# Kernel tuning notes

Hardware: AMD Instinct MI355X
Metric: run time of the kernel (lower is better)

## Reference

```python
import jax, jax.numpy as jnp
import numpy as np

B = 8           # hardcoded batchsize in the original forward
EPS = 1e-4      # scn.BatchNormalization default eps


def setup_inputs() -> dict:
    key = jax.random.key(0)
    ks = jax.random.split(key, 8)
    Nq, Nkv = 16384, 32768
    dec_in, enc_in, nf = 64, 64, 128
    nbr = jax.random.randint(ks[2], (Nq, 27), 0, Nq, dtype=jnp.int32)
    # center tap of the 3x3x3 submanifold conv is the point itself
    nbr = nbr.at[:, 13].set(jnp.arange(Nq, dtype=jnp.int32))
    return {
        "x_decoder_feat": jax.random.normal(ks[0], (Nq, dec_in), jnp.float32),
        "x_encoder_feat": jax.random.normal(ks[1], (Nkv, enc_in), jnp.float32),
        "nbr_idx": nbr,
        "W_p1": jax.random.normal(ks[3], (27, dec_in, nf), jnp.float32) * 0.05,
        "W_q": jax.random.normal(ks[4], (nf, nf), jnp.float32) * 0.05,
        "W_k": jax.random.normal(ks[5], (enc_in, nf), jnp.float32) * 0.05,
        "W_v": jax.random.normal(ks[6], (enc_in, nf), jnp.float32) * 0.05,
        "W_trans": jax.random.normal(ks[7], (nf, nf), jnp.float32) * 0.05,
        "gamma": jnp.ones((nf,), jnp.float32),
        "beta": jnp.zeros((nf,), jnp.float32),
    }


def reference(x_decoder_feat, x_encoder_feat, nbr_idx, W_p1, W_q, W_k, W_v,
              W_trans, gamma, beta):
    nf = W_q.shape[1]
    # p1: 3x3x3 submanifold conv = gather 27 neighbors, per-offset matmul, sum
    x_dec = jnp.einsum('nkc,kcf->nf', x_decoder_feat[nbr_idx], W_p1)  # [Nq,nf]
    q = (x_dec @ W_q).reshape(B, -1, nf)            # [B, nq, nf]
    k = (x_encoder_feat @ W_k).reshape(B, -1, nf)   # [B, nkv, nf]
    v = (x_encoder_feat @ W_v).reshape(B, -1, nf)
    # per-batch QK^T softmax V (no 1/sqrt(d) scaling in original)
    attn = jax.nn.softmax(jnp.einsum('bqc,bkc->bqk', q, k), axis=-1)
    x_r = jnp.einsum('bqk,bkc->bqc', attn, v).reshape(-1, nf)  # [Nq,nf]
    # trans_conv (1x1) + batchnorm (batch stats over all points)
    t = x_r @ W_trans
    mean = t.mean(axis=0)
    var = t.var(axis=0)
    bn = (t - mean) * jax.lax.rsqrt(var + EPS) * gamma + beta
    return x_dec + bn
```

## Files before the change

kernel.cpp:

```cpp
#include <hip/hip_runtime.h>
#include <math.h>

#define NQ      16384
#define NKV     32768
#define CIN     64
#define NF      128
#define NOFF    27
#define BATCH   8
#define SQ      2048
#define SKV     4096
#define BN_EPS  1e-4f
#define SPLIT   4
#define KV_PER_SPLIT (SKV / SPLIT)
#define TILES_PER_SPLIT (KV_PER_SPLIT / 64)

typedef unsigned short u16;
typedef __attribute__((ext_vector_type(4))) float f32x4;
typedef __attribute__((ext_vector_type(8))) short s16x8;

__device__ __forceinline__ u16 f2b(float x) {
    union { float f; unsigned u; } c; c.f = x;
    unsigned r = (c.u + 0x7FFFu + ((c.u >> 16) & 1u)) >> 16;
    return (u16)r;
}
__device__ __forceinline__ float b2f(u16 x) {
    union { unsigned u; float f; } c; c.u = ((unsigned)x) << 16;
    return c.f;
}
__device__ __forceinline__ void g2l16(const void* gp, void* lp) {
    __builtin_amdgcn_global_load_lds(
        (const __attribute__((address_space(1))) unsigned*)gp,
        (__attribute__((address_space(3))) unsigned*)lp, 16, 0, 0);
}

__global__ __launch_bounds__(256) void cvt_bf16_kernel(
    const float* __restrict__ src, u16* __restrict__ dst)
{
    int i = (blockIdx.x * 256 + threadIdx.x) * 4;
    float4 v = *(const float4*)(src + i);
    ushort4 o;
    o.x = f2b(v.x); o.y = f2b(v.y); o.z = f2b(v.z); o.w = f2b(v.w);
    *(ushort4*)(dst + i) = o;
}

__global__ __launch_bounds__(256) void cvt_wp1t_kernel(
    const float* __restrict__ src, u16* __restrict__ dst)
{
    int id = blockIdx.x * 256 + threadIdx.x;
    int ko = id >> 11;
    int r  = id & 2047;
    int f  = r >> 4;
    int c4 = (r & 15) * 4;
    const float* s = src + (size_t)ko * 8192 + (size_t)c4 * NF + f;
    ushort4 o;
    o.x = f2b(s[0]); o.y = f2b(s[NF]); o.z = f2b(s[2 * NF]); o.w = f2b(s[3 * NF]);
    *(ushort4*)(dst + (size_t)ko * 8192 + (size_t)f * 64 + c4) = o;
}

__global__ __launch_bounds__(256, 3) void p1conv_mfma_kernel(
    const u16* __restrict__ xf, const int* __restrict__ nbr,
    const u16* __restrict__ wt, float* __restrict__ out)
{
    __shared__ u16 As[64][64];
    __shared__ u16 Bs[64][64];
    __shared__ int nbr_s[64][28];

    const int t    = threadIdx.x;
    const int w    = t >> 6;
    const int lane = t & 63;
    const int quad = lane >> 4;
    const int l15  = lane & 15;
    const int base = blockIdx.x * 64;
    const int fh   = blockIdx.y;

    for (int i = t; i < 64 * NOFF; i += 256)
        nbr_s[i / NOFF][i % NOFF] = nbr[(size_t)base * NOFF + i];

    f32x4 oacc[4];
    #pragma unroll
    for (int n = 0; n < 4; n++) oacc[n] = (f32x4)0.f;

    __syncthreads();

    for (int ko = 0; ko < NOFF; ko++) {
        if (ko) __syncthreads();
        #pragma unroll
        for (int c = 0; c < 2; c++) {
            int row = w * 16 + c * 8 + (lane >> 3);
            int k8  = (lane & 7) ^ (row & 7);
            int nb  = nbr_s[row][ko];
            g2l16(xf + (size_t)nb * CIN + k8 * 8, &As[w * 16 + c * 8][0]);
        }
        #pragma unroll
        for (int c = 0; c < 2; c++) {
            int row = w * 16 + c * 8 + (lane >> 3);
            int k8  = (lane & 7) ^ (row & 7);
            g2l16(wt + (size_t)ko * 8192 + (size_t)(fh * 64 + row) * 64 + k8 * 8,
                  &Bs[w * 16 + c * 8][0]);
        }
        __syncthreads();

        s16x8 af[2];
        #pragma unroll
        for (int ks = 0; ks < 2; ks++) {
            int p = (ks * 4 + quad) ^ (l15 & 7);
            af[ks] = *(const s16x8*)&As[w * 16 + l15][p * 8];
        }
        #pragma unroll
        for (int nt = 0; nt < 4; nt++) {
            #pragma unroll
            for (int ks = 0; ks < 2; ks++) {
                int p = (ks * 4 + quad) ^ (l15 & 7);
                s16x8 bf = *(const s16x8*)&Bs[nt * 16 + l15][p * 8];
                oacc[nt] = __builtin_amdgcn_mfma_f32_16x16x32_bf16(af[ks], bf, oacc[nt], 0, 0, 0);
            }
        }
    }
    #pragma unroll
    for (int nt = 0; nt < 4; nt++)
        #pragma unroll
        for (int r = 0; r < 4; r++)
            out[(size_t)(base + w * 16 + quad * 4 + r) * NF + fh * 64 + nt * 16 + l15] = oacc[nt][r];
}

template<int MODE>
__global__ __launch_bounds__(256) void gemm_nf128(
    const float* __restrict__ A, const float* __restrict__ W,
    void* __restrict__ Cout, int K)
{
    __shared__ float As[64][68];
    __shared__ float Bs[64][132];
    const int t    = threadIdx.x;
    const int base = blockIdx.x * 64;
    const int ty   = t >> 4;
    const int tx   = t & 15;
    const int pl   = t >> 2;
    const int c0   = (t & 3) * 16;

    float4 acc[4][2];
    #pragma unroll
    for (int i = 0; i < 4; i++) {
        acc[i][0] = make_float4(0.f, 0.f, 0.f, 0.f);
        acc[i][1] = make_float4(0.f, 0.f, 0.f, 0.f);
    }

    for (int k0 = 0; k0 < K; k0 += 64) {
        __syncthreads();
        const float* srcA = A + (size_t)(base + pl) * K + k0 + c0;
        float4 a0 = *(const float4*)(srcA + 0);
        float4 a1 = *(const float4*)(srcA + 4);
        float4 a2 = *(const float4*)(srcA + 8);
        float4 a3 = *(const float4*)(srcA + 12);
        float4 bv[8];
        #pragma unroll
        for (int k = 0; k < 8; k++) {
            int fi = k * 256 + t;
            int r  = fi >> 5;
            int cc = (fi & 31) * 4;
            bv[k] = *(const float4*)(W + (size_t)(k0 + r) * NF + cc);
        }
        *(float4*)&As[pl][c0 + 0]  = a0;
        *(float4*)&As[pl][c0 + 4]  = a1;
        *(float4*)&As[pl][c0 + 8]  = a2;
        *(float4*)&As[pl][c0 + 12] = a3;
        #pragma unroll
        for (int k = 0; k < 8; k++) {
            int fi = k * 256 + t;
            int r  = fi >> 5;
            int cc = (fi & 31) * 4;
            *(float4*)&Bs[r][cc] = bv[k];
        }
        __syncthreads();
        #pragma unroll 4
        for (int c = 0; c < 64; c++) {
            float a[4];
            #pragma unroll
            for (int i = 0; i < 4; i++) a[i] = As[ty * 4 + i][c];
            float4 b0 = *(float4*)&Bs[c][tx * 4];
            float4 b1 = *(float4*)&Bs[c][tx * 4 + 64];
            #pragma unroll
            for (int i = 0; i < 4; i++) {
                acc[i][0].x += a[i] * b0.x; acc[i][0].y += a[i] * b0.y;
                acc[i][0].z += a[i] * b0.z; acc[i][0].w += a[i] * b0.w;
                acc[i][1].x += a[i] * b1.x; acc[i][1].y += a[i] * b1.y;
                acc[i][1].z += a[i] * b1.z; acc[i][1].w += a[i] * b1.w;
            }
        }
    }
    if (MODE == 0) {
        float* C = (float*)Cout;
        #pragma unroll
        for (int i = 0; i < 4; i++) {
            float* dst = C + (size_t)(base + ty * 4 + i) * NF;
            *(float4*)(dst + tx * 4)      = acc[i][0];
            *(float4*)(dst + tx * 4 + 64) = acc[i][1];
        }
    } else if (MODE == 1) {
        u16* C = (u16*)Cout;
        #pragma unroll
        for (int i = 0; i < 4; i++) {
            u16* dst = C + (size_t)(base + ty * 4 + i) * NF;
            #pragma unroll
            for (int h = 0; h < 2; h++) {
                const float* a = (const float*)&acc[i][h];
                ushort4 pk;
                pk.x = f2b(a[0]); pk.y = f2b(a[1]); pk.z = f2b(a[2]); pk.w = f2b(a[3]);
                *(ushort4*)(dst + tx * 4 + 64 * h) = pk;
            }
        }
    } else {
        u16* C = (u16*)Cout;
        int r0 = base + ty * 4;
        int bb = r0 >> 12;
        int kv = r0 & 4095;
        #pragma unroll
        for (int h = 0; h < 2; h++) {
            #pragma unroll
            for (int u = 0; u < 4; u++) {
                ushort4 pk;
                pk.x = f2b(((const float*)&acc[0][h])[u]);
                pk.y = f2b(((const float*)&acc[1][h])[u]);
                pk.z = f2b(((const float*)&acc[2][h])[u]);
                pk.w = f2b(((const float*)&acc[3][h])[u]);
                *(ushort4*)(C + ((size_t)(bb * NF + tx * 4 + u + 64 * h)) * SKV + kv) = pk;
            }
        }
    }
}

__global__ __launch_bounds__(256, 3) void attn_mfma_kernel(
    const u16* __restrict__ Q, const u16* __restrict__ K,
    const u16* __restrict__ Vt, u16* __restrict__ Opart,
    float* __restrict__ mpart, float* __restrict__ lpart)
{
    __shared__ u16 Ks[64][128];
    __shared__ u16 Vs[128][64];
    __shared__ u16 Ps[4][16][72];

    const int t    = threadIdx.x;
    const int b    = blockIdx.y;
    const int q0   = blockIdx.x * 64;
    const int sp   = blockIdx.z;
    const int w    = t >> 6;
    const int lane = t & 63;
    const int quad = lane >> 4;
    const int l15  = lane & 15;

    const u16* Kb  = K  + (size_t)b * SKV * NF;
    const u16* Vtb = Vt + (size_t)b * NF * SKV;

    const u16* Qp = Q + ((size_t)(b * SQ + q0 + w * 16 + l15)) * NF + quad * 8;
    s16x8 qf[4];
    #pragma unroll
    for (int ks = 0; ks < 4; ks++) qf[ks] = *(const s16x8*)(Qp + ks * 32);

    f32x4 oacc[8];
    #pragma unroll
    for (int n = 0; n < 8; n++) oacc[n] = (f32x4)0.f;
    float mrow = -1e30f, lrow = 0.f;

    const int kvbase = sp * KV_PER_SPLIT;

    for (int tile = 0; tile < TILES_PER_SPLIT; tile++) {
        int kv0 = kvbase + tile * 64;
        __syncthreads();
        #pragma unroll
        for (int c = 0; c < 4; c++) {
            int row = w * 16 + c * 4 + (lane >> 4);
            int k8  = (lane & 15) ^ (row & 15);
            g2l16(Kb + (size_t)(kv0 + row) * NF + k8 * 8, &Ks[w * 16 + c * 4][0]);
        }
        #pragma unroll
        for (int c = 0; c < 4; c++) {
            int row = w * 32 + c * 8 + (lane >> 3);
            int k8  = (lane & 7) ^ (row & 7);
            g2l16(Vtb + (size_t)row * SKV + kv0 + k8 * 8, &Vs[w * 32 + c * 8][0]);
        }
        __syncthreads();

        f32x4 sacc[4];
        #pragma unroll
        for (int c = 0; c < 4; c++) {
            sacc[c] = (f32x4)0.f;
            #pragma unroll
            for (int ks = 0; ks < 4; ks++) {
                int p = (ks * 4 + quad) ^ l15;
                s16x8 ka = *(const s16x8*)&Ks[c * 16 + l15][p * 8];
                sacc[c] = __builtin_amdgcn_mfma_f32_16x16x32_bf16(ka, qf[ks], sacc[c], 0, 0, 0);
            }
        }

        float mx = sacc[0][0];
        #pragma unroll
        for (int c = 0; c < 4; c++)
            #pragma unroll
            for (int r = 0; r < 4; r++) mx = fmaxf(mx, sacc[c][r]);
        mx = fmaxf(mx, __shfl_xor(mx, 16));
        mx = fmaxf(mx, __shfl_xor(mx, 32));
        float mnew  = fmaxf(mrow, mx);
        float alpha = __expf(mrow - mnew);
        float pv[4][4];
        float rs = 0.f;
        #pragma unroll
        for (int c = 0; c < 4; c++)
            #pragma unroll
            for (int r = 0; r < 4; r++) {
                float p = __expf(sacc[c][r] - mnew);
                pv[c][r] = p;
                rs += p;
            }
        rs += __shfl_xor(rs, 16);
        rs += __shfl_xor(rs, 32);
        lrow = lrow * alpha + rs;
        mrow = mnew;

        #pragma unroll
        for (int c = 0; c < 4; c++) {
            ushort4 pk;
            pk.x = f2b(pv[c][0]); pk.y = f2b(pv[c][1]);
            pk.z = f2b(pv[c][2]); pk.w = f2b(pv[c][3]);
            *(ushort4*)&Ps[w][l15][c * 16 + quad * 4] = pk;
        }

        #pragma unroll
        for (int n = 0; n < 8; n++) oacc[n] *= alpha;

        s16x8 pb0 = *(const s16x8*)&Ps[w][l15][quad * 8];
        s16x8 pb1 = *(const s16x8*)&Ps[w][l15][32 + quad * 8];
        #pragma unroll
        for (int mt = 0; mt < 8; mt++) {
            int p0 = quad ^ (l15 & 7);
            int p1 = (4 + quad) ^ (l15 & 7);
            s16x8 va0 = *(const s16x8*)&Vs[mt * 16 + l15][p0 * 8];
            s16x8 va1 = *(const s16x8*)&Vs[mt * 16 + l15][p1 * 8];
            oacc[mt] = __builtin_amdgcn_mfma_f32_16x16x32_bf16(va0, pb0, oacc[mt], 0, 0, 0);
            oacc[mt] = __builtin_amdgcn_mfma_f32_16x16x32_bf16(va1, pb1, oacc[mt], 0, 0, 0);
        }
    }

    int grow = b * SQ + q0 + w * 16 + l15;
    u16* Ob = Opart + (size_t)sp * NQ * NF + (size_t)grow * NF;
    #pragma unroll
    for (int mt = 0; mt < 8; mt++) {
        ushort4 ov;
        ov.x = f2b(oacc[mt][0]); ov.y = f2b(oacc[mt][1]);
        ov.z = f2b(oacc[mt][2]); ov.w = f2b(oacc[mt][3]);
        *(ushort4*)(Ob + mt * 16 + quad * 4) = ov;
    }
    if (quad == 0) {
        mpart[sp * NQ + grow] = mrow;
        lpart[sp * NQ + grow] = lrow;
    }
}

__global__ __launch_bounds__(256) void attn_merge_kernel(
    const u16* __restrict__ Opart, const float* __restrict__ mpart,
    const float* __restrict__ lpart, float* __restrict__ xr)
{
    int idx = blockIdx.x * 256 + threadIdx.x;
    int row = idx >> 5;
    int c4  = (idx & 31) * 4;
    float m[SPLIT], l[SPLIT];
    #pragma unroll
    for (int s = 0; s < SPLIT; s++) {
        m[s] = mpart[s * NQ + row];
        l[s] = lpart[s * NQ + row];
    }
    float M = m[0];
    #pragma unroll
    for (int s = 1; s < SPLIT; s++) M = fmaxf(M, m[s]);
    float L = 0.f, wgt[SPLIT];
    #pragma unroll
    for (int s = 0; s < SPLIT; s++) {
        wgt[s] = __expf(m[s] - M);
        L += l[s] * wgt[s];
    }
    float o0 = 0.f, o1 = 0.f, o2 = 0.f, o3 = 0.f;
    #pragma unroll
    for (int s = 0; s < SPLIT; s++) {
        ushort4 u = *(const ushort4*)(Opart + (size_t)s * NQ * NF + (size_t)row * NF + c4);
        o0 += wgt[s] * b2f(u.x); o1 += wgt[s] * b2f(u.y);
        o2 += wgt[s] * b2f(u.z); o3 += wgt[s] * b2f(u.w);
    }
    float inv = 1.f / L;
    float4 o = make_float4(o0 * inv, o1 * inv, o2 * inv, o3 * inv);
    *(float4*)(xr + (size_t)row * NF + c4) = o;
}

__global__ __launch_bounds__(256) void bn_stats(
    const float* __restrict__ tbuf, float* __restrict__ stats)
{
    __shared__ float red[8][128];
    __shared__ float redq[8][128];
    const int t     = threadIdx.x;
    const int tf    = t & 31;
    const int trow  = t >> 5;
    const int rbase = blockIdx.x * 128;

    float4 s  = make_float4(0.f, 0.f, 0.f, 0.f);
    float4 sq = make_float4(0.f, 0.f, 0.f, 0.f);
    #pragma unroll 4
    for (int it = 0; it < 16; it++) {
        int r = rbase + trow * 16 + it;
        float4 v = *(const float4*)(tbuf + (size_t)r * NF + tf * 4);
        s.x += v.x; s.y += v.y; s.z += v.z; s.w += v.w;
        sq.x += v.x * v.x; sq.y += v.y * v.y;
        sq.z += v.z * v.z; sq.w += v.w * v.w;
    }
    *(float4*)&red[trow][tf * 4]  = s;
    *(float4*)&redq[trow][tf * 4] = sq;
    __syncthreads();
    if (t < 128) {
        float acc = 0.f;
        #pragma unroll
        for (int i = 0; i < 8; i++) acc += red[i][t];
        atomicAdd(&stats[t], acc);
    } else {
        int f = t - 128;
        float acc = 0.f;
        #pragma unroll
        for (int i = 0; i < 8; i++) acc += redq[i][f];
        atomicAdd(&stats[128 + f], acc);
    }
}

__global__ __launch_bounds__(256) void bn_finalize(
    const float* __restrict__ tbuf, const float* __restrict__ xdec,
    const float* __restrict__ stats, const float* __restrict__ gamma,
    const float* __restrict__ beta, float* __restrict__ out)
{
    const int g = blockIdx.x * 256 + threadIdx.x;
    const int e = g * 4;
    const int f = e & (NF - 1);
    const float invN = 1.0f / (float)NQ;
    float4 tv = *(const float4*)(tbuf + e);
    float4 xv = *(const float4*)(xdec + e);
    float o[4], tt[4] = {tv.x, tv.y, tv.z, tv.w}, xx[4] = {xv.x, xv.y, xv.z, xv.w};
    #pragma unroll
    for (int u = 0; u < 4; u++) {
        float sum  = stats[f + u];
        float sumq = stats[128 + f + u];
        float mean = sum * invN;
        float var  = sumq * invN - mean * mean;
        float sc   = rsqrtf(var + BN_EPS) * gamma[f + u];
        o[u] = xx[u] + (tt[u] - mean) * sc + beta[f + u];
    }
    float4 ov = make_float4(o[0], o[1], o[2], o[3]);
    *(float4*)(out + e) = ov;
}

extern "C" void kernel_launch(void* const* d_in, const int* in_sizes, int n_in,
                              void* d_out, int out_size, void* d_ws, size_t ws_size,
                              hipStream_t stream) {
    const float* xdec_feat = (const float*)d_in[0];
    const float* xenc_feat = (const float*)d_in[1];
    const int*   nbr       = (const int*)d_in[2];
    const float* Wp1       = (const float*)d_in[3];
    const float* Wq        = (const float*)d_in[4];
    const float* Wk        = (const float*)d_in[5];
    const float* Wv        = (const float*)d_in[6];
    const float* Wt        = (const float*)d_in[7];
    const float* gamma     = (const float*)d_in[8];
    const float* beta      = (const float*)d_in[9];
    float* out = (float*)d_out;

    char* wsb = (char*)d_ws;
    const size_t MB = 1024 * 1024;
    float* xdec  = (float*)(wsb + 0);
    u16*   qbuf  = (u16*)  (wsb + 8 * MB);
    u16*   kbuf  = (u16*)  (wsb + 12 * MB);
    u16*   vt    = (u16*)  (wsb + 20 * MB);
    u16*   opart = (u16*)  (wsb + 28 * MB);
    u16*   xf_bf = (u16*)  (wsb + 28 * MB);
    u16*   wp1t  = (u16*)  (wsb + 31 * MB);
    float* mpart = (float*)(wsb + 44 * MB);
    float* lpart = (float*)(wsb + 44 * MB + 256 * 1024);
    float* stats = (float*)(wsb + 44 * MB + 512 * 1024);
    float* xr    = (float*)(wsb + 20 * MB);
    float* tbuf  = (float*)(wsb + 8 * MB);

    hipMemsetAsync(stats, 0, 256 * sizeof(float), stream);

    cvt_bf16_kernel<<<(NQ * CIN) / 1024, 256, 0, stream>>>(xdec_feat, xf_bf);
    cvt_wp1t_kernel<<<(NOFF * NF * 16) / 256, 256, 0, stream>>>(Wp1, wp1t);
    p1conv_mfma_kernel<<<dim3(NQ / 64, 2), 256, 0, stream>>>(xf_bf, nbr, wp1t, xdec);
    gemm_nf128<1><<<NQ / 64, 256, 0, stream>>>(xdec, Wq, (void*)qbuf, NF);
    gemm_nf128<1><<<NKV / 64, 256, 0, stream>>>(xenc_feat, Wk, (void*)kbuf, CIN);
    gemm_nf128<2><<<NKV / 64, 256, 0, stream>>>(xenc_feat, Wv, (void*)vt, CIN);
    attn_mfma_kernel<<<dim3(SQ / 64, BATCH, SPLIT), 256, 0, stream>>>(
        qbuf, kbuf, vt, opart, mpart, lpart);
    attn_merge_kernel<<<(NQ * 32) / 256, 256, 0, stream>>>(opart, mpart, lpart, xr);
    gemm_nf128<0><<<NQ / 64, 256, 0, stream>>>(xr, Wt, (void*)tbuf, NF);
    bn_stats<<<NQ / 128, 256, 0, stream>>>(tbuf, stats);
    bn_finalize<<<(NQ * NF) / 1024, 256, 0, stream>>>(tbuf, xdec, stats, gamma, beta, out);
}
```

Before: 227.6 us.

## Replace FP32 SIMT projection GEMMs with bf16 MFMA GEMMs on pre-transposed weights

The fp32 LDS-tiled GEMMs for the Q, K, V and trans projections are replaced by a bf16 MFMA kernel that loads A rows and transposed weights straight from global memory into fragments. Supporting this, the conv kernel also writes a bf16 copy of x_dec, the encoder features and the four weight matrices are converted to bf16, and the attention merge emits bf16. This removes the scalar FMA cost of the projections in exchange for extra conversion launches and reduced precision on x_r and x_dec inputs. Without LDS staging, the output stores become scattered 2-byte and 4-byte writes.

```diff
diff --git a/kernel.cpp b/kernel.cpp
--- a/kernel.cpp
+++ b/kernel.cpp
@@ -57,9 +57,34 @@
     *(ushort4*)(dst + (size_t)ko * 8192 + (size_t)f * 64 + c4) = o;
 }
 
+__device__ __forceinline__ void wtrans_one(
+    const float* __restrict__ src, u16* __restrict__ dst, int K, int id)
+{
+    int n  = id / (K / 4);
+    int k4 = (id % (K / 4)) * 4;
+    const float* s = src + (size_t)k4 * NF + n;
+    ushort4 o;
+    o.x = f2b(s[0]); o.y = f2b(s[NF]); o.z = f2b(s[2 * NF]); o.w = f2b(s[3 * NF]);
+    *(ushort4*)(dst + (size_t)n * K + k4) = o;
+}
+
+__global__ __launch_bounds__(256) void cvt_weights_kernel(
+    const float* __restrict__ Wq, const float* __restrict__ Wk,
+    const float* __restrict__ Wv, const float* __restrict__ Wt,
+    u16* __restrict__ wqT, u16* __restrict__ wkT,
+    u16* __restrict__ wvT, u16* __restrict__ wtT)
+{
+    int id = blockIdx.x * 256 + threadIdx.x;
+    if (id < 4096)        wtrans_one(Wq, wqT, 128, id);
+    else if (id < 6144)   wtrans_one(Wk, wkT, 64, id - 4096);
+    else if (id < 8192)   wtrans_one(Wv, wvT, 64, id - 6144);
+    else                  wtrans_one(Wt, wtT, 128, id - 8192);
+}
+
 __global__ __launch_bounds__(256, 3) void p1conv_mfma_kernel(
     const u16* __restrict__ xf, const int* __restrict__ nbr,
-    const u16* __restrict__ wt, float* __restrict__ out)
+    const u16* __restrict__ wt, float* __restrict__ out,
+    u16* __restrict__ outb)
 {
     __shared__ u16 As[64][64];
     __shared__ u16 Bs[64][64];
@@ -119,111 +144,68 @@
     #pragma unroll
     for (int nt = 0; nt < 4; nt++)
         #pragma unroll
-        for (int r = 0; r < 4; r++)
-            out[(size_t)(base + w * 16 + quad * 4 + r) * NF + fh * 64 + nt * 16 + l15] = oacc[nt][r];
-}
-
-template<int MODE>
-__global__ __launch_bounds__(256) void gemm_nf128(
-    const float* __restrict__ A, const float* __restrict__ W,
-    void* __restrict__ Cout, int K)
-{
-    __shared__ float As[64][68];
-    __shared__ float Bs[64][132];
+        for (int r = 0; r < 4; r++) {
+            size_t idx = (size_t)(base + w * 16 + quad * 4 + r) * NF + fh * 64 + nt * 16 + l15;
+            out[idx]  = oacc[nt][r];
+            outb[idx] = f2b(oacc[nt][r]);
+        }
+}
+
+template<int MODE, int K>
+__global__ __launch_bounds__(256) void gemm_mfma(
+    const u16* __restrict__ A, const u16* __restrict__ WT,
+    void* __restrict__ out)
+{
     const int t    = threadIdx.x;
-    const int base = blockIdx.x * 64;
-    const int ty   = t >> 4;
-    const int tx   = t & 15;
-    const int pl   = t >> 2;
-    const int c0   = (t & 3) * 16;
-
-    float4 acc[4][2];
-    #pragma unroll
-    for (int i = 0; i < 4; i++) {
-        acc[i][0] = make_float4(0.f, 0.f, 0.f, 0.f);
-        acc[i][1] = make_float4(0.f, 0.f, 0.f, 0.f);
-    }
-
-    for (int k0 = 0; k0 < K; k0 += 64) {
-        __syncthreads();
-        const float* srcA = A + (size_t)(base + pl) * K + k0 + c0;
-        float4 a0 = *(const float4*)(srcA + 0);
-        float4 a1 = *(const float4*)(srcA + 4);
-        float4 a2 = *(const float4*)(srcA + 8);
-        float4 a3 = *(const float4*)(srcA + 12);
-        float4 bv[8];
-        #pragma unroll
-        for (int k = 0; k < 8; k++) {
-            int fi = k * 256 + t;
-            int r  = fi >> 5;
-            int cc = (fi & 31) * 4;
-            bv[k] = *(const float4*)(W + (size_t)(k0 + r) * NF + cc);
-        }
-        *(float4*)&As[pl][c0 + 0]  = a0;
-        *(float4*)&As[pl][c0 + 4]  = a1;
-        *(float4*)&As[pl][c0 + 8]  = a2;
-        *(float4*)&As[pl][c0 + 12] = a3;
-        #pragma unroll
-        for (int k = 0; k < 8; k++) {
-            int fi = k * 256 + t;
-            int r  = fi >> 5;
-            int cc = (fi & 31) * 4;
-            *(float4*)&Bs[r][cc] = bv[k];
-        }
-        __syncthreads();
-        #pragma unroll 4
-        for (int c = 0; c < 64; c++) {
-            float a[4];
-            #pragma unroll
-            for (int i = 0; i < 4; i++) a[i] = As[ty * 4 + i][c];
-            float4 b0 = *(float4*)&Bs[c][tx * 4];
-            float4 b1 = *(float4*)&Bs[c][tx * 4 + 64];
-            #pragma unroll
-            for (int i = 0; i < 4; i++) {
-                acc[i][0].x += a[i] * b0.x; acc[i][0].y += a[i] * b0.y;
-                acc[i][0].z += a[i] * b0.z; acc[i][0].w += a[i] * b0.w;
-                acc[i][1].x += a[i] * b1.x; acc[i][1].y += a[i] * b1.y;
-                acc[i][1].z += a[i] * b1.z; acc[i][1].w += a[i] * b1.w;
-            }
-        }
-    }
+    const int w    = t >> 6;
+    const int lane = t & 63;
+    const int quad = lane >> 4;
+    const int l15  = lane & 15;
+    const int m0   = blockIdx.x * 64 + w * 16;
+    constexpr int KF = K / 32;
+
+    s16x8 af[KF];
+    const u16* Ap = A + (size_t)(m0 + l15) * K + quad * 8;
+    #pragma unroll
+    for (int ks = 0; ks < KF; ks++) af[ks] = *(const s16x8*)(Ap + ks * 32);
+
+    f32x4 oacc[8];
+    #pragma unroll
+    for (int nt = 0; nt < 8; nt++) {
+        oacc[nt] = (f32x4)0.f;
+        const u16* Wp = WT + (size_t)(nt * 16 + l15) * K + quad * 8;
+        #pragma unroll
+        for (int ks = 0; ks < KF; ks++) {
+            s16x8 bf = *(const s16x8*)(Wp + ks * 32);
+            oacc[nt] = __builtin_amdgcn_mfma_f32_16x16x32_bf16(af[ks], bf, oacc[nt], 0, 0, 0);
+        }
+    }
+
     if (MODE == 0) {
-        float* C = (float*)Cout;
-        #pragma unroll
-        for (int i = 0; i < 4; i++) {
-            float* dst = C + (size_t)(base + ty * 4 + i) * NF;
-            *(float4*)(dst + tx * 4)      = acc[i][0];
-            *(float4*)(dst + tx * 4 + 64) = acc[i][1];
-        }
+        float* C = (float*)out;
+        #pragma unroll
+        for (int nt = 0; nt < 8; nt++)
+            #pragma unroll
+            for (int r = 0; r < 4; r++)
+                C[(size_t)(m0 + quad * 4 + r) * NF + nt * 16 + l15] = oacc[nt][r];
     } else if (MODE == 1) {
-        u16* C = (u16*)Cout;
-        #pragma unroll
-        for (int i = 0; i < 4; i++) {
-            u16* dst = C + (size_t)(base + ty * 4 + i) * NF;
-            #pragma unroll
-            for (int h = 0; h < 2; h++) {
-                const float* a = (const float*)&acc[i][h];
-                ushort4 pk;
-                pk.x = f2b(a[0]); pk.y = f2b(a[1]); pk.z = f2b(a[2]); pk.w = f2b(a[3]);
-                *(ushort4*)(dst + tx * 4 + 64 * h) = pk;
-            }
-        }
+        u16* C = (u16*)out;
+        #pragma unroll
+        for (int nt = 0; nt < 8; nt++)
+            #pragma unroll
+            for (int r = 0; r < 4; r++)
+                C[(size_t)(m0 + quad * 4 + r) * NF + nt * 16 + l15] = f2b(oacc[nt][r]);
     } else {
-        u16* C = (u16*)Cout;
-        int r0 = base + ty * 4;
-        int bb = r0 >> 12;
-        int kv = r0 & 4095;
-        #pragma unroll
-        for (int h = 0; h < 2; h++) {
-            #pragma unroll
-            for (int u = 0; u < 4; u++) {
-                ushort4 pk;
-                pk.x = f2b(((const float*)&acc[0][h])[u]);
-                pk.y = f2b(((const float*)&acc[1][h])[u]);
-                pk.z = f2b(((const float*)&acc[2][h])[u]);
-                pk.w = f2b(((const float*)&acc[3][h])[u]);
-                *(ushort4*)(C + ((size_t)(bb * NF + tx * 4 + u + 64 * h)) * SKV + kv) = pk;
-            }
+        u16* C = (u16*)out;
+        int m  = m0 + quad * 4;
+        int bb = m >> 12;
+        int kv = m & 4095;
+        #pragma unroll
+        for (int nt = 0; nt < 8; nt++) {
+            ushort4 pk;
+            pk.x = f2b(oacc[nt][0]); pk.y = f2b(oacc[nt][1]);
+            pk.z = f2b(oacc[nt][2]); pk.w = f2b(oacc[nt][3]);
+            *(ushort4*)(C + (size_t)(bb * NF + nt * 16 + l15) * SKV + kv) = pk;
         }
     }
 }
@@ -355,7 +337,7 @@
 
 __global__ __launch_bounds__(256) void attn_merge_kernel(
     const u16* __restrict__ Opart, const float* __restrict__ mpart,
-    const float* __restrict__ lpart, float* __restrict__ xr)
+    const float* __restrict__ lpart, u16* __restrict__ xrb)
 {
     int idx = blockIdx.x * 256 + threadIdx.x;
     int row = idx >> 5;
@@ -383,8 +365,10 @@
         o2 += wgt[s] * b2f(u.z); o3 += wgt[s] * b2f(u.w);
     }
     float inv = 1.f / L;
-    float4 o = make_float4(o0 * inv, o1 * inv, o2 * inv, o3 * inv);
-    *(float4*)(xr + (size_t)row * NF + c4) = o;
+    ushort4 ob;
+    ob.x = f2b(o0 * inv); ob.y = f2b(o1 * inv);
+    ob.z = f2b(o2 * inv); ob.w = f2b(o3 * inv);
+    *(ushort4*)(xrb + (size_t)row * NF + c4) = ob;
 }
 
 __global__ __launch_bounds__(256) void bn_stats(
@@ -466,31 +450,39 @@
 
     char* wsb = (char*)d_ws;
     const size_t MB = 1024 * 1024;
-    float* xdec  = (float*)(wsb + 0);
-    u16*   qbuf  = (u16*)  (wsb + 8 * MB);
-    u16*   kbuf  = (u16*)  (wsb + 12 * MB);
-    u16*   vt    = (u16*)  (wsb + 20 * MB);
-    u16*   opart = (u16*)  (wsb + 28 * MB);
-    u16*   xf_bf = (u16*)  (wsb + 28 * MB);
-    u16*   wp1t  = (u16*)  (wsb + 31 * MB);
-    float* mpart = (float*)(wsb + 44 * MB);
-    float* lpart = (float*)(wsb + 44 * MB + 256 * 1024);
-    float* stats = (float*)(wsb + 44 * MB + 512 * 1024);
-    float* xr    = (float*)(wsb + 20 * MB);
-    float* tbuf  = (float*)(wsb + 8 * MB);
+    float* xdec   = (float*)(wsb + 0);
+    u16*   qbuf   = (u16*)  (wsb + 8 * MB);
+    u16*   kbuf   = (u16*)  (wsb + 12 * MB);
+    u16*   vt     = (u16*)  (wsb + 20 * MB);
+    u16*   opart  = (u16*)  (wsb + 28 * MB);
+    u16*   xf_bf  = (u16*)  (wsb + 28 * MB);
+    u16*   xenc_b = (u16*)  (wsb + 30 * MB);
+    u16*   xdec_b = (u16*)  (wsb + 34 * MB);
+    u16*   wp1t   = (u16*)  (wsb + 44 * MB);
+    u16*   wqT    = (u16*)  (wsb + 44 * MB + 512 * 1024);
+    u16*   wkT    = (u16*)  (wsb + 44 * MB + 512 * 1024 + 32768);
+    u16*   wvT    = (u16*)  (wsb + 44 * MB + 512 * 1024 + 49152);
+    u16*   wtT    = (u16*)  (wsb + 44 * MB + 512 * 1024 + 65536);
+    float* mpart  = (float*)(wsb + 45 * MB);
+    float* lpart  = (float*)(wsb + 45 * MB + 256 * 1024);
+    float* stats  = (float*)(wsb + 45 * MB + 512 * 1024);
+    u16*   xr_bf  = (u16*)  (wsb + 20 * MB);
+    float* tbuf   = (float*)(wsb + 8 * MB);
 
     hipMemsetAsync(stats, 0, 256 * sizeof(float), stream);
 
     cvt_bf16_kernel<<<(NQ * CIN) / 1024, 256, 0, stream>>>(xdec_feat, xf_bf);
+    cvt_bf16_kernel<<<(NKV * CIN) / 1024, 256, 0, stream>>>(xenc_feat, xenc_b);
     cvt_wp1t_kernel<<<(NOFF * NF * 16) / 256, 256, 0, stream>>>(Wp1, wp1t);
-    p1conv_mfma_kernel<<<dim3(NQ / 64, 2), 256, 0, stream>>>(xf_bf, nbr, wp1t, xdec);
-    gemm_nf128<1><<<NQ / 64, 256, 0, stream>>>(xdec, Wq, (void*)qbuf, NF);
-    gemm_nf128<1><<<NKV / 64, 256, 0, stream>>>(xenc_feat, Wk, (void*)kbuf, CIN);
-    gemm_nf128<2><<<NKV / 64, 256, 0, stream>>>(xenc_feat, Wv, (void*)vt, CIN);
+    cvt_weights_kernel<<<48, 256, 0, stream>>>(Wq, Wk, Wv, Wt, wqT, wkT, wvT, wtT);
+    p1conv_mfma_kernel<<<dim3(NQ / 64, 2), 256, 0, stream>>>(xf_bf, nbr, wp1t, xdec, xdec_b);
+    gemm_mfma<1, 128><<<NQ / 64, 256, 0, stream>>>(xdec_b, wqT, (void*)qbuf);
+    gemm_mfma<1, 64><<<NKV / 64, 256, 0, stream>>>(xenc_b, wkT, (void*)kbuf);
+    gemm_mfma<2, 64><<<NKV / 64, 256, 0, stream>>>(xenc_b, wvT, (void*)vt);
     attn_mfma_kernel<<<dim3(SQ / 64, BATCH, SPLIT), 256, 0, stream>>>(
         qbuf, kbuf, vt, opart, mpart, lpart);
-    attn_merge_kernel<<<(NQ * 32) / 256, 256, 0, stream>>>(opart, mpart, lpart, xr);
-    gemm_nf128<0><<<NQ / 64, 256, 0, stream>>>(xr, Wt, (void*)tbuf, NF);
+    attn_merge_kernel<<<(NQ * 32) / 256, 256, 0, stream>>>(opart, mpart, lpart, xr_bf);
+    gemm_mfma<0, 128><<<NQ / 64, 256, 0, stream>>>(xr_bf, wtT, (void*)tbuf);
     bn_stats<<<NQ / 128, 256, 0, stream>>>(tbuf, stats);
     bn_finalize<<<(NQ * NF) / 1024, 256, 0, stream>>>(tbuf, xdec, stats, gamma, beta, out);
 }
```

Result: faster. 214.9 us (-5.6%).
